# Kernel tuning notes

Hardware: AMD Instinct MI355X
Metric: run time of the kernel (lower is better)

The kernel has to match this reference:

```python
import jax, jax.numpy as jnp
import numpy as np

ALPHA = 0.2  # LeakyReLU negative slope
NEG_INF = -9e15


def setup_inputs() -> dict:
    key = jax.random.key(0)
    k1, k2, k3, k4 = jax.random.split(key, 4)
    B, N, F_in, F_out = 8, 2048, 512, 256
    h = jax.random.normal(k1, (B, N, F_in), dtype=jnp.float32)
    adj = jax.random.randint(k2, (B, N, N), 0, 2, dtype=jnp.int32)
    W = jax.random.normal(k3, (F_in, F_out), dtype=jnp.float32) * (1.414 / np.sqrt(F_in))
    a = jax.random.normal(k4, (2 * F_out, 1), dtype=jnp.float32) * (1.414 / np.sqrt(2 * F_out))
    return {"h": h, "adj": adj, "W": W, "a": a}


def reference(h, adj, W, a):
    # Wh: [B, N, F_out]
    Wh = jnp.matmul(h, W)
    F_out = W.shape[1]
    a1 = a[:F_out, 0]   # [F_out] -> source (row i) part
    a2 = a[F_out:, 0]   # [F_out] -> target (col j) part
    # e[b,i,j] = leakyrelu(Wh[b,i]@a1 + Wh[b,j]@a2)  (decomposed concat-attention)
    f1 = jnp.einsum('bnf,f->bn', Wh, a1)  # [B, N]
    f2 = jnp.einsum('bnf,f->bn', Wh, a2)  # [B, N]
    e = f1[:, :, None] + f2[:, None, :]   # [B, N, N]
    e = jnp.where(e > 0, e, ALPHA * e)    # LeakyReLU
    e = jnp.where(adj > 0, e, NEG_INF)
    attention = jax.nn.softmax(e, axis=2)
    # dropout p=0.0 / eval mode: identity
    h_prime = jnp.matmul(attention, Wh)   # [B, N, F_out]
    return jax.nn.elu(h_prime)            # concat=True branch
```

## Files before the change

### kernel.cpp

```cpp
#include <hip/hip_runtime.h>
#include <hip/hip_bf16.h>

#define GAT_ALPHA 0.2f

typedef short bf16x8 __attribute__((ext_vector_type(8)));
typedef float f32x4 __attribute__((ext_vector_type(4)));

__device__ __forceinline__ unsigned f2bf_u(float x) {
  union { float f; unsigned u; } v; v.f = x;
  return (v.u + 0x7fffu + ((v.u >> 16) & 1u)) >> 16;
}
__device__ __forceinline__ unsigned short f2bf(float x) { return (unsigned short)f2bf_u(x); }

__global__ void k_wt(const float* __restrict__ W, unsigned short* __restrict__ WT) {
  int kb = blockIdx.x * 8;
  int f = threadIdx.x;
  bf16x8 o;
#pragma unroll
  for (int i = 0; i < 8; ++i) o[i] = (short)f2bf(W[(kb + i) * 256 + f]);
  *reinterpret_cast<bf16x8*>(WT + f * 512 + kb) = o;
}

__global__ __launch_bounds__(512, 2) void k_gemm1(
    const float* __restrict__ h, const unsigned short* __restrict__ WT,
    const float* __restrict__ avec,
    unsigned short* __restrict__ WhT,
    float* __restrict__ E1p, float* __restrict__ E1n,
    float* __restrict__ E2p, float* __restrict__ E2n)
{
  const int bx = blockIdx.x;
  const int b = bx & 7, ng = bx >> 3;
  const int n0 = ng * 64;
  const int t = threadIdx.x;
  const int lane = t & 63, w = t >> 6;
  const int mtg = w >> 1, ntp = w & 1;
  const int l15 = lane & 15, q = lane >> 4;

  __shared__ float f1acc[64], f2acc[64];
  if (t < 64) { f1acc[t] = 0.f; f2acc[t] = 0.f; }

  f32x4 acc[4][2];
#pragma unroll
  for (int i = 0; i < 4; ++i)
#pragma unroll
    for (int j = 0; j < 2; ++j) acc[i][j] = (f32x4){0.f, 0.f, 0.f, 0.f};

  const size_t hrow0 = ((size_t)(b * 2048 + n0 + ntp * 32 + l15)) * 512;

#pragma unroll 2
  for (int k0 = 0; k0 < 512; k0 += 32) {
    bf16x8 af[4];
#pragma unroll
    for (int mt = 0; mt < 4; ++mt) {
      int fr = mtg * 64 + mt * 16 + l15;
      af[mt] = *reinterpret_cast<const bf16x8*>(WT + fr * 512 + k0 + q * 8);
    }
    bf16x8 bfr[2];
#pragma unroll
    for (int nt = 0; nt < 2; ++nt) {
      const float* hp = h + hrow0 + (size_t)nt * (16 * 512) + k0 + q * 8;
      float4 x0 = *reinterpret_cast<const float4*>(hp);
      float4 x1 = *reinterpret_cast<const float4*>(hp + 4);
      bf16x8 bb;
      bb[0] = (short)f2bf(x0.x); bb[1] = (short)f2bf(x0.y);
      bb[2] = (short)f2bf(x0.z); bb[3] = (short)f2bf(x0.w);
      bb[4] = (short)f2bf(x1.x); bb[5] = (short)f2bf(x1.y);
      bb[6] = (short)f2bf(x1.z); bb[7] = (short)f2bf(x1.w);
      bfr[nt] = bb;
    }
#pragma unroll
    for (int mt = 0; mt < 4; ++mt)
#pragma unroll
      for (int nt = 0; nt < 2; ++nt)
        acc[mt][nt] = __builtin_amdgcn_mfma_f32_16x16x32_bf16(af[mt], bfr[nt], acc[mt][nt], 0, 0, 0);
  }

  float s1[2] = {0.f, 0.f}, s2[2] = {0.f, 0.f};
#pragma unroll
  for (int mt = 0; mt < 4; ++mt) {
#pragma unroll
    for (int nt = 0; nt < 2; ++nt) {
      int n = n0 + ntp * 32 + nt * 16 + l15;
#pragma unroll
      for (int r = 0; r < 4; ++r) {
        int f = mtg * 64 + mt * 16 + q * 4 + r;
        float v = acc[mt][nt][r];
        WhT[(size_t)(b * 256 + f) * 2048 + n] = f2bf(v);
        s1[nt] += v * avec[f];
        s2[nt] += v * avec[256 + f];
      }
    }
  }
  __syncthreads();
#pragma unroll
  for (int nt = 0; nt < 2; ++nt) {
    float a1 = s1[nt], a2 = s2[nt];
    a1 += __shfl_xor(a1, 16); a1 += __shfl_xor(a1, 32);
    a2 += __shfl_xor(a2, 16); a2 += __shfl_xor(a2, 32);
    if (q == 0) {
      atomicAdd(&f1acc[ntp * 32 + nt * 16 + l15], a1);
      atomicAdd(&f2acc[ntp * 32 + nt * 16 + l15], a2);
    }
  }
  __syncthreads();
  if (t < 64) {
    int n = b * 2048 + n0 + t;
    float f1 = f1acc[t], f2 = f2acc[t];
    E1p[n] = __expf(f1);
    E1n[n] = __expf(GAT_ALPHA * f1);
    E2p[n] = __expf(f2);
    E2n[n] = __expf(GAT_ALPHA * f2);
  }
}

__global__ __launch_bounds__(512, 2) void k_gat(
    const int* __restrict__ adj, const unsigned short* __restrict__ WhT,
    const float* __restrict__ E1p, const float* __restrict__ E1n,
    const float* __restrict__ E2p, const float* __restrict__ E2n,
    float* __restrict__ out)
{
  const int bx = blockIdx.x;
  const int b = bx & 7, ig = bx >> 3;
  const int i0 = ig * 64;
  const int t = threadIdx.x;
  const int lane = t & 63, w = t >> 6;
  const int l15 = lane & 15, q = lane >> 4;
  const int crow = t >> 5;
  const int ccol = (t & 31) * 4;

  __shared__ unsigned short Pb[2][64][136];
  __shared__ float den_l[64];

  float e1p[4], e1n[4];
#pragma unroll
  for (int p = 0; p < 4; ++p) {
    int r = b * 2048 + i0 + crow + 16 * p;
    e1p[p] = E1p[r]; e1n[p] = E1n[r];
  }
  float den[4] = {0.f, 0.f, 0.f, 0.f};

  const size_t adjbase = ((size_t)(b * 2048 + i0 + crow)) * 2048 + ccol;
  const int e2base = b * 2048 + ccol;

  f32x4 acc[4][2];
#pragma unroll
  for (int i = 0; i < 4; ++i)
#pragma unroll
    for (int j = 0; j < 2; ++j) acc[i][j] = (f32x4){0.f, 0.f, 0.f, 0.f};

  int4 av[4]; float4 e2pv, e2nv;
#pragma unroll
  for (int p = 0; p < 4; ++p)
    av[p] = *reinterpret_cast<const int4*>(adj + adjbase + (size_t)(16 * p) * 2048);
  e2pv = *reinterpret_cast<const float4*>(E2p + e2base);
  e2nv = *reinterpret_cast<const float4*>(E2n + e2base);
  {
    unsigned short* wb = &Pb[0][0][0];
#pragma unroll
    for (int p = 0; p < 4; ++p) {
      float p0 = fmaxf(e1p[p] * e2pv.x, e1n[p] * e2nv.x); p0 = av[p].x ? p0 : 0.f;
      float p1 = fmaxf(e1p[p] * e2pv.y, e1n[p] * e2nv.y); p1 = av[p].y ? p1 : 0.f;
      float p2 = fmaxf(e1p[p] * e2pv.z, e1n[p] * e2nv.z); p2 = av[p].z ? p2 : 0.f;
      float p3 = fmaxf(e1p[p] * e2pv.w, e1n[p] * e2nv.w); p3 = av[p].w ? p3 : 0.f;
      den[p] += (p0 + p1) + (p2 + p3);
      uint2 pk;
      pk.x = f2bf_u(p0) | (f2bf_u(p1) << 16);
      pk.y = f2bf_u(p2) | (f2bf_u(p3) << 16);
      *reinterpret_cast<uint2*>(wb + (crow + 16 * p) * 136 + ccol) = pk;
    }
  }

  for (int c = 0; c < 16; ++c) {
    __syncthreads();
    int4 nav[4]; float4 ne2p, ne2n;
    if (c < 15) {
      int j0 = (c + 1) * 128;
#pragma unroll
      for (int p = 0; p < 4; ++p)
        nav[p] = *reinterpret_cast<const int4*>(adj + adjbase + (size_t)(16 * p) * 2048 + j0);
      ne2p = *reinterpret_cast<const float4*>(E2p + e2base + j0);
      ne2n = *reinterpret_cast<const float4*>(E2n + e2base + j0);
    }
    const unsigned short* pbuf = &Pb[c & 1][0][0];
#pragma unroll
    for (int ks = 0; ks < 4; ++ks) {
      bf16x8 afr[4];
#pragma unroll
      for (int rt = 0; rt < 4; ++rt)
        afr[rt] = *reinterpret_cast<const bf16x8*>(pbuf + (rt * 16 + l15) * 136 + ks * 32 + q * 8);
      bf16x8 bfr[2];
#pragma unroll
      for (int ct = 0; ct < 2; ++ct) {
        int f = w * 32 + ct * 16 + l15;
        bfr[ct] = *reinterpret_cast<const bf16x8*>(
            WhT + (size_t)(b * 256 + f) * 2048 + c * 128 + ks * 32 + q * 8);
      }
#pragma unroll
      for (int rt = 0; rt < 4; ++rt)
#pragma unroll
        for (int ct = 0; ct < 2; ++ct)
          acc[rt][ct] = __builtin_amdgcn_mfma_f32_16x16x32_bf16(afr[rt], bfr[ct], acc[rt][ct], 0, 0, 0);
    }
    if (c < 15) {
      unsigned short* wb = &Pb[(c + 1) & 1][0][0];
#pragma unroll
      for (int p = 0; p < 4; ++p) {
        float p0 = fmaxf(e1p[p] * ne2p.x, e1n[p] * ne2n.x); p0 = nav[p].x ? p0 : 0.f;
        float p1 = fmaxf(e1p[p] * ne2p.y, e1n[p] * ne2n.y); p1 = nav[p].y ? p1 : 0.f;
        float p2 = fmaxf(e1p[p] * ne2p.z, e1n[p] * ne2n.z); p2 = nav[p].z ? p2 : 0.f;
        float p3 = fmaxf(e1p[p] * ne2p.w, e1n[p] * ne2n.w); p3 = nav[p].w ? p3 : 0.f;
        den[p] += (p0 + p1) + (p2 + p3);
        uint2 pk;
        pk.x = f2bf_u(p0) | (f2bf_u(p1) << 16);
        pk.y = f2bf_u(p2) | (f2bf_u(p3) << 16);
        *reinterpret_cast<uint2*>(wb + (crow + 16 * p) * 136 + ccol) = pk;
      }
    }
  }

#pragma unroll
  for (int p = 0; p < 4; ++p) {
    float s = den[p];
    s += __shfl_xor(s, 1); s += __shfl_xor(s, 2); s += __shfl_xor(s, 4);
    s += __shfl_xor(s, 8); s += __shfl_xor(s, 16);
    if ((lane & 31) == 0) den_l[(t >> 5) + 16 * p] = s;
  }
  __syncthreads();

#pragma unroll
  for (int rt = 0; rt < 4; ++rt) {
#pragma unroll
    for (int r = 0; r < 4; ++r) {
      int row = rt * 16 + q * 4 + r;
      float dinv = 1.0f / den_l[row];
      size_t obase = ((size_t)(b * 2048 + i0 + row)) * 256;
#pragma unroll
      for (int ct = 0; ct < 2; ++ct) {
        int f = w * 32 + ct * 16 + l15;
        float v = acc[rt][ct][r] * dinv;
        v = v > 0.f ? v : (__expf(v) - 1.f);
        out[obase + f] = v;
      }
    }
  }
}

extern "C" void kernel_launch(void* const* d_in, const int* in_sizes, int n_in,
                              void* d_out, int out_size, void* d_ws, size_t ws_size,
                              hipStream_t stream) {
  const float* h   = (const float*)d_in[0];
  const int*   adj = (const int*)d_in[1];
  const float* W   = (const float*)d_in[2];
  const float* a   = (const float*)d_in[3];
  float* out = (float*)d_out;

  char* ws = (char*)d_ws;
  unsigned short* WhT = (unsigned short*)ws;
  unsigned short* WT  = (unsigned short*)(ws + 8388608);
  float* E1p = (float*)(ws + 8388608 + 262144);
  float* E1n = E1p + 16384;
  float* E2p = E1n + 16384;
  float* E2n = E2p + 16384;

  k_wt<<<dim3(64), dim3(256), 0, stream>>>(W, WT);
  k_gemm1<<<dim3(256), dim3(512), 0, stream>>>(h, WT, a, WhT, E1p, E1n, E2p, E2n);
  k_gat<<<dim3(256), dim3(512), 0, stream>>>(adj, WhT, E1p, E1n, E2p, E2n, out);
}
```

Measured before the change: 282.9 us.

## Split GAT neighbor dimension across blocks, add finalize kernel, restage gemm1 output

The attention kernel can now split the neighbor (j) range in two across twice as many blocks. Each block writes unnormalized numerators and partial denominators, and a new finalize kernel sums the halves, normalizes and applies ELU. The P tile in shared memory is stored in MFMA fragment order, and each thread builds 8-wide fragments. gemm1 now uses smaller 256-thread blocks over 32 rows and stages its WhT output through shared memory for coalesced stores. This adds an extra pass over 16MB of partials, and the split path only runs when the workspace is large enough.

```diff
diff --git a/kernel.cpp b/kernel.cpp
--- a/kernel.cpp
+++ b/kernel.cpp
@@ -21,7 +21,7 @@
   *reinterpret_cast<bf16x8*>(WT + f * 512 + kb) = o;
 }
 
-__global__ __launch_bounds__(512, 2) void k_gemm1(
+__global__ __launch_bounds__(256, 4) void k_gemm1(
     const float* __restrict__ h, const unsigned short* __restrict__ WT,
     const float* __restrict__ avec,
     unsigned short* __restrict__ WhT,
@@ -30,14 +30,14 @@
 {
   const int bx = blockIdx.x;
   const int b = bx & 7, ng = bx >> 3;
-  const int n0 = ng * 64;
+  const int n0 = ng * 32;
   const int t = threadIdx.x;
   const int lane = t & 63, w = t >> 6;
-  const int mtg = w >> 1, ntp = w & 1;
   const int l15 = lane & 15, q = lane >> 4;
 
-  __shared__ float f1acc[64], f2acc[64];
-  if (t < 64) { f1acc[t] = 0.f; f2acc[t] = 0.f; }
+  __shared__ __align__(16) unsigned short Wt[256 * 36];
+  __shared__ float f1a[32], f2a[32];
+  if (t < 32) { f1a[t] = 0.f; f2a[t] = 0.f; }
 
   f32x4 acc[4][2];
 #pragma unroll
@@ -45,20 +45,18 @@
 #pragma unroll
     for (int j = 0; j < 2; ++j) acc[i][j] = (f32x4){0.f, 0.f, 0.f, 0.f};
 
-  const size_t hrow0 = ((size_t)(b * 2048 + n0 + ntp * 32 + l15)) * 512;
+  const size_t hbase = ((size_t)(b * 2048 + n0)) * 512;
 
 #pragma unroll 2
   for (int k0 = 0; k0 < 512; k0 += 32) {
     bf16x8 af[4];
 #pragma unroll
-    for (int mt = 0; mt < 4; ++mt) {
-      int fr = mtg * 64 + mt * 16 + l15;
-      af[mt] = *reinterpret_cast<const bf16x8*>(WT + fr * 512 + k0 + q * 8);
-    }
+    for (int mt = 0; mt < 4; ++mt)
+      af[mt] = *reinterpret_cast<const bf16x8*>(WT + (w * 64 + mt * 16 + l15) * 512 + k0 + q * 8);
     bf16x8 bfr[2];
 #pragma unroll
     for (int nt = 0; nt < 2; ++nt) {
-      const float* hp = h + hrow0 + (size_t)nt * (16 * 512) + k0 + q * 8;
+      const float* hp = h + hbase + (size_t)(nt * 16 + l15) * 512 + k0 + q * 8;
       float4 x0 = *reinterpret_cast<const float4*>(hp);
       float4 x1 = *reinterpret_cast<const float4*>(hp + 4);
       bf16x8 bb;
@@ -80,32 +78,39 @@
   for (int mt = 0; mt < 4; ++mt) {
 #pragma unroll
     for (int nt = 0; nt < 2; ++nt) {
-      int n = n0 + ntp * 32 + nt * 16 + l15;
 #pragma unroll
       for (int r = 0; r < 4; ++r) {
-        int f = mtg * 64 + mt * 16 + q * 4 + r;
+        int f = w * 64 + mt * 16 + q * 4 + r;
         float v = acc[mt][nt][r];
-        WhT[(size_t)(b * 256 + f) * 2048 + n] = f2bf(v);
+        Wt[f * 36 + nt * 16 + l15] = f2bf(v);
         s1[nt] += v * avec[f];
         s2[nt] += v * avec[256 + f];
       }
     }
   }
+#pragma unroll
+  for (int nt = 0; nt < 2; ++nt) {
+    s1[nt] += __shfl_xor(s1[nt], 16); s1[nt] += __shfl_xor(s1[nt], 32);
+    s2[nt] += __shfl_xor(s2[nt], 16); s2[nt] += __shfl_xor(s2[nt], 32);
+  }
   __syncthreads();
-#pragma unroll
-  for (int nt = 0; nt < 2; ++nt) {
-    float a1 = s1[nt], a2 = s2[nt];
-    a1 += __shfl_xor(a1, 16); a1 += __shfl_xor(a1, 32);
-    a2 += __shfl_xor(a2, 16); a2 += __shfl_xor(a2, 32);
-    if (q == 0) {
-      atomicAdd(&f1acc[ntp * 32 + nt * 16 + l15], a1);
-      atomicAdd(&f2acc[ntp * 32 + nt * 16 + l15], a2);
-    }
+  if (q == 0) {
+#pragma unroll
+    for (int nt = 0; nt < 2; ++nt) {
+      atomicAdd(&f1a[nt * 16 + l15], s1[nt]);
+      atomicAdd(&f2a[nt * 16 + l15], s2[nt]);
+    }
+  }
+#pragma unroll
+  for (int i = 0; i < 8; ++i) {
+    int f = i * 32 + (t >> 3), g = t & 7;
+    uint2 v = *reinterpret_cast<const uint2*>(Wt + f * 36 + g * 4);
+    *reinterpret_cast<uint2*>(WhT + (size_t)(b * 256 + f) * 2048 + n0 + g * 4) = v;
   }
   __syncthreads();
-  if (t < 64) {
+  if (t < 32) {
     int n = b * 2048 + n0 + t;
-    float f1 = f1acc[t], f2 = f2acc[t];
+    float f1 = f1a[t], f2 = f2a[t];
     E1p[n] = __expf(f1);
     E1n[n] = __expf(GAT_ALPHA * f1);
     E2p[n] = __expf(f2);
@@ -113,34 +118,58 @@
   }
 }
 
-__global__ __launch_bounds__(512, 2) void k_gat(
+__device__ __forceinline__ void build_frag(
+    unsigned short* dst, int4 alo, int4 ahi, float e1p, float e1n,
+    float4 epl, float4 eph, float4 enl, float4 enh, float& den)
+{
+  float p0 = alo.x ? fmaxf(e1p * epl.x, e1n * enl.x) : 0.f;
+  float p1 = alo.y ? fmaxf(e1p * epl.y, e1n * enl.y) : 0.f;
+  float p2 = alo.z ? fmaxf(e1p * epl.z, e1n * enl.z) : 0.f;
+  float p3 = alo.w ? fmaxf(e1p * epl.w, e1n * enl.w) : 0.f;
+  float p4 = ahi.x ? fmaxf(e1p * eph.x, e1n * enh.x) : 0.f;
+  float p5 = ahi.y ? fmaxf(e1p * eph.y, e1n * enh.y) : 0.f;
+  float p6 = ahi.z ? fmaxf(e1p * eph.z, e1n * enh.z) : 0.f;
+  float p7 = ahi.w ? fmaxf(e1p * eph.w, e1n * enh.w) : 0.f;
+  den += ((p0 + p1) + (p2 + p3)) + ((p4 + p5) + (p6 + p7));
+  uint4 pk;
+  pk.x = f2bf_u(p0) | (f2bf_u(p1) << 16);
+  pk.y = f2bf_u(p2) | (f2bf_u(p3) << 16);
+  pk.z = f2bf_u(p4) | (f2bf_u(p5) << 16);
+  pk.w = f2bf_u(p6) | (f2bf_u(p7) << 16);
+  *reinterpret_cast<uint4*>(dst) = pk;
+}
+
+template<int JS>
+__global__ __launch_bounds__(512, 4) void k_gat(
     const int* __restrict__ adj, const unsigned short* __restrict__ WhT,
     const float* __restrict__ E1p, const float* __restrict__ E1n,
     const float* __restrict__ E2p, const float* __restrict__ E2n,
-    float* __restrict__ out)
+    float* __restrict__ num0, float* __restrict__ num1, float* __restrict__ denp)
 {
+  const int NCH = 16 / JS;
   const int bx = blockIdx.x;
-  const int b = bx & 7, ig = bx >> 3;
+  const int b = bx & 7;
+  const int rest = bx >> 3;
+  const int js = (JS == 2) ? (rest & 1) : 0;
+  const int ig = (JS == 2) ? (rest >> 1) : rest;
   const int i0 = ig * 64;
+  const int j00 = js * (NCH * 128);
+
   const int t = threadIdx.x;
   const int lane = t & 63, w = t >> 6;
   const int l15 = lane & 15, q = lane >> 4;
-  const int crow = t >> 5;
-  const int ccol = (t & 31) * 4;
-
-  __shared__ unsigned short Pb[2][64][136];
+  const int m = t & 15, qk = (t >> 4) & 3, pp = t >> 6;
+  const int rt0 = pp >> 2, ks = pp & 3;
+  const int r0 = rt0 * 16 + m, r1 = r0 + 32;
+  const int cb = ks * 32 + qk * 8;
+
+  __shared__ __align__(16) unsigned short Pb[2][8192];
   __shared__ float den_l[64];
-
-  float e1p[4], e1n[4];
-#pragma unroll
-  for (int p = 0; p < 4; ++p) {
-    int r = b * 2048 + i0 + crow + 16 * p;
-    e1p[p] = E1p[r]; e1n[p] = E1n[r];
-  }
-  float den[4] = {0.f, 0.f, 0.f, 0.f};
-
-  const size_t adjbase = ((size_t)(b * 2048 + i0 + crow)) * 2048 + ccol;
-  const int e2base = b * 2048 + ccol;
+  if (t < 64) den_l[t] = 0.f;
+
+  const float e1p0 = E1p[b * 2048 + i0 + r0], e1n0 = E1n[b * 2048 + i0 + r0];
+  const float e1p1 = E1p[b * 2048 + i0 + r1], e1n1 = E1n[b * 2048 + i0 + r1];
+  float d0 = 0.f, d1 = 0.f;
 
   f32x4 acc[4][2];
 #pragma unroll
@@ -148,100 +177,113 @@
 #pragma unroll
     for (int j = 0; j < 2; ++j) acc[i][j] = (f32x4){0.f, 0.f, 0.f, 0.f};
 
-  int4 av[4]; float4 e2pv, e2nv;
-#pragma unroll
-  for (int p = 0; p < 4; ++p)
-    av[p] = *reinterpret_cast<const int4*>(adj + adjbase + (size_t)(16 * p) * 2048);
-  e2pv = *reinterpret_cast<const float4*>(E2p + e2base);
-  e2nv = *reinterpret_cast<const float4*>(E2n + e2base);
+  const size_t adj0 = ((size_t)(b * 2048 + i0 + r0)) * 2048 + j00 + cb;
+  const size_t adj1 = adj0 + (size_t)32 * 2048;
+  const int e2b = b * 2048 + j00 + cb;
+  const unsigned short* Wb = WhT + (size_t)(b * 256 + w * 32) * 2048 + j00;
+
   {
-    unsigned short* wb = &Pb[0][0][0];
-#pragma unroll
-    for (int p = 0; p < 4; ++p) {
-      float p0 = fmaxf(e1p[p] * e2pv.x, e1n[p] * e2nv.x); p0 = av[p].x ? p0 : 0.f;
-      float p1 = fmaxf(e1p[p] * e2pv.y, e1n[p] * e2nv.y); p1 = av[p].y ? p1 : 0.f;
-      float p2 = fmaxf(e1p[p] * e2pv.z, e1n[p] * e2nv.z); p2 = av[p].z ? p2 : 0.f;
-      float p3 = fmaxf(e1p[p] * e2pv.w, e1n[p] * e2nv.w); p3 = av[p].w ? p3 : 0.f;
-      den[p] += (p0 + p1) + (p2 + p3);
-      uint2 pk;
-      pk.x = f2bf_u(p0) | (f2bf_u(p1) << 16);
-      pk.y = f2bf_u(p2) | (f2bf_u(p3) << 16);
-      *reinterpret_cast<uint2*>(wb + (crow + 16 * p) * 136 + ccol) = pk;
-    }
-  }
-
-  for (int c = 0; c < 16; ++c) {
+    int4 a0l = *reinterpret_cast<const int4*>(adj + adj0);
+    int4 a0h = *reinterpret_cast<const int4*>(adj + adj0 + 4);
+    int4 a1l = *reinterpret_cast<const int4*>(adj + adj1);
+    int4 a1h = *reinterpret_cast<const int4*>(adj + adj1 + 4);
+    float4 epl = *reinterpret_cast<const float4*>(E2p + e2b);
+    float4 eph = *reinterpret_cast<const float4*>(E2p + e2b + 4);
+    float4 enl = *reinterpret_cast<const float4*>(E2n + e2b);
+    float4 enh = *reinterpret_cast<const float4*>(E2n + e2b + 4);
+    build_frag(&Pb[0][(pp * 64 + lane) * 8], a0l, a0h, e1p0, e1n0, epl, eph, enl, enh, d0);
+    build_frag(&Pb[0][((pp + 8) * 64 + lane) * 8], a1l, a1h, e1p1, e1n1, epl, eph, enl, enh, d1);
+  }
+
+  for (int c = 0; c < NCH; ++c) {
     __syncthreads();
-    int4 nav[4]; float4 ne2p, ne2n;
-    if (c < 15) {
-      int j0 = (c + 1) * 128;
-#pragma unroll
-      for (int p = 0; p < 4; ++p)
-        nav[p] = *reinterpret_cast<const int4*>(adj + adjbase + (size_t)(16 * p) * 2048 + j0);
-      ne2p = *reinterpret_cast<const float4*>(E2p + e2base + j0);
-      ne2n = *reinterpret_cast<const float4*>(E2n + e2base + j0);
-    }
-    const unsigned short* pbuf = &Pb[c & 1][0][0];
-#pragma unroll
-    for (int ks = 0; ks < 4; ++ks) {
+    int4 na0l, na0h, na1l, na1h;
+    if (c + 1 < NCH) {
+      int o = (c + 1) * 128;
+      na0l = *reinterpret_cast<const int4*>(adj + adj0 + o);
+      na0h = *reinterpret_cast<const int4*>(adj + adj0 + o + 4);
+      na1l = *reinterpret_cast<const int4*>(adj + adj1 + o);
+      na1h = *reinterpret_cast<const int4*>(adj + adj1 + o + 4);
+    }
+    bf16x8 bfr[2][4];
+#pragma unroll
+    for (int ct = 0; ct < 2; ++ct)
+#pragma unroll
+      for (int k2 = 0; k2 < 4; ++k2)
+        bfr[ct][k2] = *reinterpret_cast<const bf16x8*>(
+            Wb + (size_t)(ct * 16 + l15) * 2048 + c * 128 + k2 * 32 + q * 8);
+    const unsigned short* pb = &Pb[c & 1][0];
+#pragma unroll
+    for (int k2 = 0; k2 < 4; ++k2) {
       bf16x8 afr[4];
 #pragma unroll
       for (int rt = 0; rt < 4; ++rt)
-        afr[rt] = *reinterpret_cast<const bf16x8*>(pbuf + (rt * 16 + l15) * 136 + ks * 32 + q * 8);
-      bf16x8 bfr[2];
-#pragma unroll
-      for (int ct = 0; ct < 2; ++ct) {
-        int f = w * 32 + ct * 16 + l15;
-        bfr[ct] = *reinterpret_cast<const bf16x8*>(
-            WhT + (size_t)(b * 256 + f) * 2048 + c * 128 + ks * 32 + q * 8);
-      }
+        afr[rt] = *reinterpret_cast<const bf16x8*>(pb + ((rt * 4 + k2) * 64 + lane) * 8);
 #pragma unroll
       for (int rt = 0; rt < 4; ++rt)
 #pragma unroll
         for (int ct = 0; ct < 2; ++ct)
-          acc[rt][ct] = __builtin_amdgcn_mfma_f32_16x16x32_bf16(afr[rt], bfr[ct], acc[rt][ct], 0, 0, 0);
-    }
-    if (c < 15) {
-      unsigned short* wb = &Pb[(c + 1) & 1][0][0];
-#pragma unroll
-      for (int p = 0; p < 4; ++p) {
-        float p0 = fmaxf(e1p[p] * ne2p.x, e1n[p] * ne2n.x); p0 = nav[p].x ? p0 : 0.f;
-        float p1 = fmaxf(e1p[p] * ne2p.y, e1n[p] * ne2n.y); p1 = nav[p].y ? p1 : 0.f;
-        float p2 = fmaxf(e1p[p] * ne2p.z, e1n[p] * ne2n.z); p2 = nav[p].z ? p2 : 0.f;
-        float p3 = fmaxf(e1p[p] * ne2p.w, e1n[p] * ne2n.w); p3 = nav[p].w ? p3 : 0.f;
-        den[p] += (p0 + p1) + (p2 + p3);
-        uint2 pk;
-        pk.x = f2bf_u(p0) | (f2bf_u(p1) << 16);
-        pk.y = f2bf_u(p2) | (f2bf_u(p3) << 16);
-        *reinterpret_cast<uint2*>(wb + (crow + 16 * p) * 136 + ccol) = pk;
-      }
-    }
-  }
-
-#pragma unroll
-  for (int p = 0; p < 4; ++p) {
-    float s = den[p];
-    s += __shfl_xor(s, 1); s += __shfl_xor(s, 2); s += __shfl_xor(s, 4);
-    s += __shfl_xor(s, 8); s += __shfl_xor(s, 16);
-    if ((lane & 31) == 0) den_l[(t >> 5) + 16 * p] = s;
+          acc[rt][ct] = __builtin_amdgcn_mfma_f32_16x16x32_bf16(afr[rt], bfr[ct][k2], acc[rt][ct], 0, 0, 0);
+    }
+    if (c + 1 < NCH) {
+      int o = (c + 1) * 128;
+      float4 epl = *reinterpret_cast<const float4*>(E2p + e2b + o);
+      float4 eph = *reinterpret_cast<const float4*>(E2p + e2b + o + 4);
+      float4 enl = *reinterpret_cast<const float4*>(E2n + e2b + o);
+      float4 enh = *reinterpret_cast<const float4*>(E2n + e2b + o + 4);
+      unsigned short* wb = &Pb[(c + 1) & 1][0];
+      build_frag(wb + (pp * 64 + lane) * 8, na0l, na0h, e1p0, e1n0, epl, eph, enl, enh, d0);
+      build_frag(wb + ((pp + 8) * 64 + lane) * 8, na1l, na1h, e1p1, e1n1, epl, eph, enl, enh, d1);
+    }
+  }
+
+  d0 += __shfl_xor(d0, 16); d0 += __shfl_xor(d0, 32);
+  d1 += __shfl_xor(d1, 16); d1 += __shfl_xor(d1, 32);
+  if (lane < 16) {
+    atomicAdd(&den_l[r0], d0);
+    atomicAdd(&den_l[r1], d1);
   }
   __syncthreads();
 
+  float* nout = (JS == 2 && js == 1) ? num1 : num0;
 #pragma unroll
   for (int rt = 0; rt < 4; ++rt) {
 #pragma unroll
     for (int r = 0; r < 4; ++r) {
       int row = rt * 16 + q * 4 + r;
-      float dinv = 1.0f / den_l[row];
-      size_t obase = ((size_t)(b * 2048 + i0 + row)) * 256;
-#pragma unroll
-      for (int ct = 0; ct < 2; ++ct) {
-        int f = w * 32 + ct * 16 + l15;
-        float v = acc[rt][ct][r] * dinv;
-        v = v > 0.f ? v : (__expf(v) - 1.f);
-        out[obase + f] = v;
-      }
-    }
+      size_t ob = ((size_t)(b * 2048 + i0 + row)) * 256 + w * 32;
+#pragma unroll
+      for (int ct = 0; ct < 2; ++ct)
+        nout[ob + ct * 16 + l15] = acc[rt][ct][r];
+    }
+  }
+  if (t < 64) denp[js * 16384 + b * 2048 + i0 + t] = den_l[t];
+}
+
+template<int JS>
+__global__ __launch_bounds__(256) void k_fin(
+    const float* __restrict__ n0p, const float* __restrict__ n1p,
+    const float* __restrict__ denp, float* __restrict__ out)
+{
+  int i = blockIdx.x * 256 + threadIdx.x;
+#pragma unroll
+  for (int rep = 0; rep < 2; ++rep) {
+    int i4 = i + rep * 524288;
+    float4 v = reinterpret_cast<const float4*>(n0p)[i4];
+    float dn = denp[i4 >> 6];
+    if (JS == 2) {
+      float4 u = reinterpret_cast<const float4*>(n1p)[i4];
+      v.x += u.x; v.y += u.y; v.z += u.z; v.w += u.w;
+      dn += denp[16384 + (i4 >> 6)];
+    }
+    float id = 1.0f / dn;
+    float4 o;
+    float x;
+    x = v.x * id; o.x = x > 0.f ? x : (__expf(x) - 1.f);
+    x = v.y * id; o.y = x > 0.f ? x : (__expf(x) - 1.f);
+    x = v.z * id; o.z = x > 0.f ? x : (__expf(x) - 1.f);
+    x = v.w * id; o.w = x > 0.f ? x : (__expf(x) - 1.f);
+    reinterpret_cast<float4*>(out)[i4] = o;
   }
 }
 
@@ -257,12 +299,23 @@
   char* ws = (char*)d_ws;
   unsigned short* WhT = (unsigned short*)ws;
   unsigned short* WT  = (unsigned short*)(ws + 8388608);
-  float* E1p = (float*)(ws + 8388608 + 262144);
-  float* E1n = E1p + 16384;
-  float* E2p = E1n + 16384;
-  float* E2n = E2p + 16384;
+  float* E1p  = (float*)(ws + 8388608 + 262144);
+  float* E1n  = E1p + 16384;
+  float* E2p  = E1n + 16384;
+  float* E2n  = E2p + 16384;
+  float* denp = E2n + 16384;
+  float* num1 = denp + 2 * 16384;
+
+  const size_t need2 = 8388608ull + 262144 + 4 * 65536 + 131072 + 16777216;
+  const bool js2 = (ws_size >= need2);
 
   k_wt<<<dim3(64), dim3(256), 0, stream>>>(W, WT);
-  k_gemm1<<<dim3(256), dim3(512), 0, stream>>>(h, WT, a, WhT, E1p, E1n, E2p, E2n);
-  k_gat<<<dim3(256), dim3(512), 0, stream>>>(adj, WhT, E1p, E1n, E2p, E2n, out);
-}
+  k_gemm1<<<dim3(512), dim3(256), 0, stream>>>(h, WT, a, WhT, E1p, E1n, E2p, E2n);
+  if (js2) {
+    k_gat<2><<<dim3(512), dim3(512), 0, stream>>>(adj, WhT, E1p, E1n, E2p, E2n, out, num1, denp);
+    k_fin<2><<<dim3(2048), dim3(256), 0, stream>>>(out, num1, denp, out);
+  } else {
+    k_gat<1><<<dim3(256), dim3(512), 0, stream>>>(adj, WhT, E1p, E1n, E2p, E2n, out, num1, denp);
+    k_fin<1><<<dim3(2048), dim3(256), 0, stream>>>(out, num1, denp, out);
+  }
+}
```

Result: no change. 284.6 us (+0.6%).
